# Kernel optimization log

Hardware: AMD Instinct MI355X
Metric: run time of the kernel (lower is better)

## Reference

```python
import jax, jax.numpy as jnp
import numpy as np

B, N, D_MODEL, H = 2, 512, 256, 8
DH, DS, DE = 8, 8, 8          # hyperbolic / spherical / euclidean component dims
HEAD = D_MODEL // H           # 32
HALF = HEAD // 2              # 16 rope frequencies
KAPPA_S = 1.0                 # spherical curvature
EPS = 1e-6


def setup_inputs() -> dict:
    key = jax.random.key(0)
    ks = jax.random.split(key, 10)
    h = jax.random.normal(ks[0], (B, N, D_MODEL), jnp.float32)
    # manifold coords: hyperbolic part inside Poincare ball, spherical part on unit sphere
    xh = 0.3 * jnp.tanh(jax.random.normal(ks[1], (B, N, DH), jnp.float32))
    xs_raw = jax.random.normal(ks[2], (B, N, DS), jnp.float32)
    xs = xs_raw / jnp.linalg.norm(xs_raw, axis=-1, keepdims=True)
    xe = jax.random.normal(ks[3], (B, N, DE), jnp.float32)
    x = jnp.concatenate([xh, xs, xe], axis=-1)
    def lin(k):
        return 0.05 * jax.random.normal(k, (D_MODEL, D_MODEL), jnp.float32)
    inp = dict(
        h=h, x=x,
        Wq=lin(ks[4]), bq=jnp.zeros((D_MODEL,), jnp.float32),
        Wk=lin(ks[5]), bk=jnp.zeros((D_MODEL,), jnp.float32),
        Wv=lin(ks[6]), bv=jnp.zeros((D_MODEL,), jnp.float32),
        Wo=lin(ks[7]), bo=jnp.zeros((D_MODEL,), jnp.float32),
        w_kernel=jnp.ones((H, 3), jnp.float32),   # torch init: ones(num_heads, num_comp)
        beta=jnp.ones((H,), jnp.float32),
        edge_bias=0.1 * jax.random.normal(ks[8], (B, 1, N, N), jnp.float32),
        node_mask=jnp.ones((B, N), bool),
    )
    return inp


def _pairwise_geometry(x):
    """Returns dh (B,N,N), sdot (B,N,N), de2 (B,N,N), dist (B,N,N)."""
    xh, xs, xe = x[..., :DH], x[..., DH:DH + DS], x[..., DH + DS:]
    # hyperbolic: Poincare-ball distance arccosh(1 + 2|a-b|^2 / ((1-|a|^2)(1-|b|^2)))
    dh2_num = jnp.sum((xh[:, :, None, :] - xh[:, None, :, :]) ** 2, -1)
    one_m = 1.0 - jnp.sum(xh * xh, -1)                               # (B,N)
    arg = 1.0 + 2.0 * dh2_num / (one_m[:, :, None] * one_m[:, None, :])
    dh = jnp.arccosh(jnp.maximum(arg, 1.0 + EPS))
    # spherical: arccos of dot (unit vectors); raw dot kept for the kernel term
    sdot = jnp.einsum('bnd,bmd->bnm', xs, xs)
    ds = jnp.arccos(jnp.clip(sdot, -1.0 + EPS, 1.0 - EPS)) / np.sqrt(KAPPA_S)
    # euclidean: squared distance (kernel uses -d^2; product dist uses d^2)
    de2 = jnp.sum((xe[:, :, None, :] - xe[:, None, :, :]) ** 2, -1)
    dist = jnp.sqrt(dh * dh + ds * ds + de2)
    return dh, sdot, de2, dist


def reference(h, x, Wq, bq, Wk, bk, Wv, bv, Wo, bo, w_kernel, beta, edge_bias, node_mask):
    scale = 1.0 / np.sqrt(HEAD)
    rope_freq = jnp.exp(-np.log(10000.0) * jnp.arange(HALF, dtype=jnp.float32) / HALF)

    def heads(t):  # (B,N,D) -> (B,H,N,head)
        return t.reshape(B, N, H, HEAD).transpose(0, 2, 1, 3)

    Q = heads(h @ Wq.T + bq)
    K = heads(h @ Wk.T + bk)
    V = heads(h @ Wv.T + bv)

    dh, sdot, de2, dist = _pairwise_geometry(x)

    # M-RoPE: rotate Q by pairwise angle theta_ij = omega * d_M(x_i, x_j)
    theta = dist[..., None] * rope_freq                  # (B,N,N,half)
    cos_t = jnp.cos(theta)[:, None]                      # (B,1,N,N,half)
    sin_t = jnp.sin(theta)[:, None]
    q1, q2 = Q[..., 0::2], Q[..., 1::2]                  # (B,H,N,half)
    k1, k2 = K[..., 0::2], K[..., 1::2]
    qk_same = q1[:, :, :, None, :] * k1[:, :, None, :, :] + q2[:, :, :, None, :] * k2[:, :, None, :, :]
    qk_cross = q1[:, :, :, None, :] * k2[:, :, None, :, :] - q2[:, :, :, None, :] * k1[:, :, None, :, :]
    attn = (cos_t * qk_same + sin_t * qk_cross).sum(-1) * scale   # (B,H,N,N)

    # geodesic kernel bias: per-component kernels [H:-d_H, S:k*a.b, E:-|a-b|^2]
    kernel_stack = jnp.stack([-dh, KAPPA_S * sdot, -de2], axis=-1)  # (B,N,N,3)
    geo = jnp.einsum('hc,bnmc->bhnm', w_kernel, kernel_stack)
    attn = attn + beta[None, :, None, None] * geo + edge_bias

    attn = jnp.where(node_mask[:, None, None, :], attn, -jnp.inf)
    p = jax.nn.softmax(attn, axis=-1)
    out = jnp.einsum('bhnm,bhmd->bhnd', p, V).transpose(0, 2, 1, 3).reshape(B, N, D_MODEL)
    return out @ Wo.T + bo
```

## Files before the change

### kernel.cpp

```cpp
#include <hip/hip_runtime.h>

#define N_TOK 512
#define NH 8

typedef __attribute__((ext_vector_type(8))) short short8;
typedef __attribute__((ext_vector_type(4))) short short4v;
typedef __attribute__((ext_vector_type(4))) float f32x4;

__device__ __forceinline__ unsigned short f2bf(float f) {
    union { float f; unsigned u; } v; v.f = f;
    return (unsigned short)((v.u + 0x7FFF + ((v.u >> 16) & 1)) >> 16);
}

__global__ __launch_bounds__(256) void gemm_qkv_mfma(
    const float* __restrict__ A,
    const float* __restrict__ Wq, const float* __restrict__ Wk, const float* __restrict__ Wv,
    const float* __restrict__ bq, const float* __restrict__ bk, const float* __restrict__ bv,
    float* __restrict__ Qb, float* __restrict__ KR, float* __restrict__ Vb)
{
    const int bx = blockIdx.x;
    const int t = threadIdx.x;
    const int z = bx >> 8, rem = bx & 255;
    const int m0 = (rem >> 3) * 32, n0 = (rem & 7) * 32;
    const float* W    = (z == 0) ? Wq : (z == 1) ? Wk : Wv;
    const float* bias = (z == 0) ? bq : (z == 1) ? bk : bv;

    __shared__ short As[32][264];
    __shared__ short Ws[32][264];

    #pragma unroll
    for (int r = 0; r < 8; ++r) {
        int idx = t + 256 * r;
        int row = idx >> 6, c4 = (idx & 63) * 4;
        float4 a = *(const float4*)&A[(m0 + row) * 256 + c4];
        short4v pa = {(short)f2bf(a.x), (short)f2bf(a.y), (short)f2bf(a.z), (short)f2bf(a.w)};
        *(short4v*)&As[row][c4] = pa;
        float4 w = *(const float4*)&W[(n0 + row) * 256 + c4];
        short4v pw = {(short)f2bf(w.x), (short)f2bf(w.y), (short)f2bf(w.z), (short)f2bf(w.w)};
        *(short4v*)&Ws[row][c4] = pw;
    }
    __syncthreads();

    const int w = t >> 6, lane = t & 63;
    const int wm = (w >> 1) * 16, wn = (w & 1) * 16;
    const int frow = lane & 15, kq = lane >> 4;

    f32x4 acc = {0.f, 0.f, 0.f, 0.f};
    #pragma unroll
    for (int k0 = 0; k0 < 8; ++k0) {
        short8 af = *(const short8*)&As[wm + frow][k0 * 32 + kq * 8];
        short8 wf = *(const short8*)&Ws[wn + frow][k0 * 32 + kq * 8];
        if (z == 1) acc = __builtin_amdgcn_mfma_f32_16x16x32_bf16(wf, af, acc, 0, 0, 0);
        else        acc = __builtin_amdgcn_mfma_f32_16x16x32_bf16(af, wf, acc, 0, 0, 0);
    }
    const int col = lane & 15, rq = (lane >> 4) * 4;
    if (z == 1) {
        int tok = m0 + wm + col;
        int bb = tok >> 9, j = tok & 511;
        #pragma unroll
        for (int r = 0; r < 4; ++r) {
            int d = n0 + wn + rq + r;
            int h = d >> 5, dd = d & 31, f = dd >> 1, r2 = dd & 1;
            KR[((size_t)bb * 128 + h * 16 + f) * 1024 + j * 2 + r2] = acc[r] + bias[d];
        }
    } else {
        float* C = (z == 0) ? Qb : Vb;
        float bsv = bias[n0 + wn + col];
        #pragma unroll
        for (int r = 0; r < 4; ++r)
            C[(m0 + wm + rq + r) * 256 + n0 + wn + col] = acc[r] + bsv;
    }
}

__global__ __launch_bounds__(256) void geo_kernel(
    const float* __restrict__ x, float* __restrict__ geo)
{
    const int j0 = blockIdx.x * 256;
    const int i  = blockIdx.y;
    const int b  = blockIdx.z;
    const int t  = threadIdx.x;

    __shared__ float xls[256 * 25];
    const float4* xsrc = (const float4*)(x + ((size_t)b * N_TOK + j0) * 24);
    #pragma unroll
    for (int r = 0; r < 6; ++r) {
        int idx = t + 256 * r;
        float4 v = xsrc[idx];
        int row = idx / 6, c = (idx % 6) * 4;
        float* dst = &xls[row * 25 + c];
        dst[0] = v.x; dst[1] = v.y; dst[2] = v.z; dst[3] = v.w;
    }
    const float* xi = x + ((size_t)b * N_TOK + i) * 24;
    float onemi = 1.0f;
    #pragma unroll
    for (int k = 0; k < 8; ++k) onemi -= xi[k] * xi[k];
    __syncthreads();

    const float* xr = &xls[t * 25];
    float dh2 = 0.f, oj = 0.f, sd = 0.f, de2 = 0.f;
    #pragma unroll
    for (int k = 0; k < 8; ++k) { float xj = xr[k]; float d = xi[k] - xj; dh2 += d * d; oj += xj * xj; }
    #pragma unroll
    for (int k = 0; k < 8; ++k) sd += xi[8 + k] * xr[8 + k];
    #pragma unroll
    for (int k = 0; k < 8; ++k) { float d = xi[16 + k] - xr[16 + k]; de2 += d * d; }
    float arg = 1.0f + 2.0f * dh2 / (onemi * (1.0f - oj));
    arg = fmaxf(arg, 1.0f + 1e-6f);
    float dh = __logf(arg + sqrtf(arg * arg - 1.0f));
    float sdc = fminf(fmaxf(sd, -1.0f + 1e-6f), 1.0f - 1e-6f);
    float dsp = acosf(sdc);
    float dist = sqrtf(dh * dh + dsp * dsp + de2);

    size_t idx = ((size_t)b * N_TOK + i) * N_TOK + j0 + t;
    float4 o; o.x = dh; o.y = sd; o.z = de2; o.w = dist * 0.15915494309189535f;
    *(float4*)&geo[idx * 4] = o;
}

__global__ __launch_bounds__(256, 4) void attn_kernel(
    const float* __restrict__ Q, const float* __restrict__ KR, const float* __restrict__ V,
    const float* __restrict__ geo, const float* __restrict__ eb,
    const float* __restrict__ wker, const float* __restrict__ beta,
    float* __restrict__ num, float* __restrict__ den)
{
    const float FRQ[16] = {
        1.0f, 0.5623413251903491f, 0.31622776601683794f, 0.17782794100389228f,
        0.1f, 0.05623413251903491f, 0.031622776601683794f, 0.017782794100389228f,
        0.01f, 0.005623413251903491f, 0.0031622776601683794f, 0.0017782794100389228f,
        0.001f, 0.0005623413251903491f, 0.00031622776601683795f, 0.00017782794100389228f};

    const int t = threadIdx.x;
    const int lane = t & 63;
    const int wv = t >> 6;
    const int wid = blockIdx.x * 4 + wv;
    const int b  = __builtin_amdgcn_readfirstlane(wid >> 12);
    const int h  = __builtin_amdgcn_readfirstlane((wid >> 9) & 7);
    const int ip = __builtin_amdgcn_readfirstlane((wid >> 1) & 255);
    const int jh = __builtin_amdgcn_readfirstlane(wid & 1);
    const int i0 = ip * 2;

    __shared__ float es[4][2][128];

    const float* q0p = Q + ((size_t)b * N_TOK + i0) * 256 + h * 32;
    const float* q1p = q0p + 256;
    const float wk0 = wker[h * 3 + 0], wk1 = wker[h * 3 + 1], wk2 = wker[h * 3 + 2];
    const float bet = beta[h];
    const float scale = 0.17677669529663687f;

    const size_t gbase = ((size_t)b * N_TOK + i0) * N_TOK;
    const float* kbase = KR + ((size_t)b * 128 + h * 16) * 1024;

    float dsum[2] = {0.f, 0.f};
    float acc[2][4] = {{0.f,0.f,0.f,0.f},{0.f,0.f,0.f,0.f}};
    const int jsub = lane >> 3, dq = lane & 7;

    for (int tile = 0; tile < 2; ++tile) {
        const int j0 = jh * 256 + tile * 128;
        float2 gdh[2], gsd[2], gde[2], gds[2];
        #pragma unroll
        for (int ii = 0; ii < 2; ++ii) {
            size_t gi = (gbase + (size_t)ii * N_TOK + j0 + 2 * lane) * 4;
            float4 g0 = *(const float4*)&geo[gi];
            float4 g1 = *(const float4*)&geo[gi + 4];
            gdh[ii] = make_float2(g0.x, g1.x);
            gsd[ii] = make_float2(g0.y, g1.y);
            gde[ii] = make_float2(g0.z, g1.z);
            gds[ii] = make_float2(g0.w, g1.w);
        }
        float dot[2][2] = {{0.f, 0.f}, {0.f, 0.f}};
        #pragma unroll
        for (int fg = 0; fg < 2; ++fg) {
            float4 kv[8];
            #pragma unroll
            for (int fl = 0; fl < 8; ++fl)
                kv[fl] = *(const float4*)&kbase[(size_t)(fg * 8 + fl) * 1024 + (j0 + 2 * lane) * 2];
            #pragma unroll
            for (int fl = 0; fl < 8; ++fl) {
                const int f = fg * 8 + fl;
                const float frq = FRQ[f];
                float4 kk = kv[fl];
                #pragma unroll
                for (int ii = 0; ii < 2; ++ii) {
                    const float* qp = ii ? q1p : q0p;
                    float q1 = qp[f * 2], q2 = qp[f * 2 + 1];
                    float r0 = gds[ii].x * frq; r0 -= floorf(r0);
                    float r1 = gds[ii].y * frq; r1 -= floorf(r1);
                    float s0 = __builtin_amdgcn_sinf(r0), c0 = __builtin_amdgcn_cosf(r0);
                    float s1 = __builtin_amdgcn_sinf(r1), c1 = __builtin_amdgcn_cosf(r1);
                    float t1 = q1 * kk.x + q2 * kk.y;
                    float t2 = q1 * kk.y - q2 * kk.x;
                    dot[ii][0] += c0 * t1 + s0 * t2;
                    t1 = q1 * kk.z + q2 * kk.w;
                    t2 = q1 * kk.w - q2 * kk.z;
                    dot[ii][1] += c1 * t1 + s1 * t2;
                }
            }
        }
        #pragma unroll
        for (int ii = 0; ii < 2; ++ii) {
            float2 e2 = *(const float2*)&eb[((size_t)b * N_TOK + i0 + ii) * N_TOK + j0 + 2 * lane];
            float bias0 = bet * (wk1 * gsd[ii].x - wk0 * gdh[ii].x - wk2 * gde[ii].x) + e2.x;
            float bias1 = bet * (wk1 * gsd[ii].y - wk0 * gdh[ii].y - wk2 * gde[ii].y) + e2.y;
            float e0 = __expf(dot[ii][0] * scale + bias0);
            float e1 = __expf(dot[ii][1] * scale + bias1);
            dsum[ii] += e0 + e1;
            *(float2*)&es[wv][ii][2 * lane] = make_float2(e0, e1);
        }
        {
            const float* vp = V + ((size_t)b * N_TOK + j0 + jsub) * 256 + h * 32 + dq * 4;
            #pragma unroll
            for (int it = 0; it < 16; ++it) {
                float4 v4 = *(const float4*)&vp[(size_t)it * 8 * 256];
                int j = it * 8 + jsub;
                float e0 = es[wv][0][j], e1 = es[wv][1][j];
                acc[0][0] += e0 * v4.x; acc[0][1] += e0 * v4.y;
                acc[0][2] += e0 * v4.z; acc[0][3] += e0 * v4.w;
                acc[1][0] += e1 * v4.x; acc[1][1] += e1 * v4.y;
                acc[1][2] += e1 * v4.z; acc[1][3] += e1 * v4.w;
            }
        }
    }

    #pragma unroll
    for (int ii = 0; ii < 2; ++ii) {
        float v = dsum[ii];
        v += __shfl_xor(v, 1);  v += __shfl_xor(v, 2);  v += __shfl_xor(v, 4);
        v += __shfl_xor(v, 8);  v += __shfl_xor(v, 16); v += __shfl_xor(v, 32);
        dsum[ii] = v;
    }
    #pragma unroll
    for (int ii = 0; ii < 2; ++ii)
        #pragma unroll
        for (int dd = 0; dd < 4; ++dd) {
            float a = acc[ii][dd];
            a += __shfl_xor(a, 8); a += __shfl_xor(a, 16); a += __shfl_xor(a, 32);
            acc[ii][dd] = a;
        }
    float* denp = den + (size_t)jh * 8192;
    if (lane == 0) {
        denp[((size_t)b * N_TOK + i0) * 8 + h]     = dsum[0];
        denp[((size_t)b * N_TOK + i0 + 1) * 8 + h] = dsum[1];
    }
    if (jsub == 0) {
        #pragma unroll
        for (int ii = 0; ii < 2; ++ii) {
            float4 o; o.x = acc[ii][0]; o.y = acc[ii][1]; o.z = acc[ii][2]; o.w = acc[ii][3];
            *(float4*)&num[(size_t)jh * 262144 + ((size_t)b * N_TOK + i0 + ii) * 256 + h * 32 + dq * 4] = o;
        }
    }
}

__global__ __launch_bounds__(256) void gemm_out_mfma(
    const float* __restrict__ num, const float* __restrict__ den,
    const float* __restrict__ Wo, const float* __restrict__ bo, float* __restrict__ out)
{
    const int t = threadIdx.x;
    const int m0 = (blockIdx.x >> 3) * 32, n0 = (blockIdx.x & 7) * 32;

    __shared__ short As[32][264];
    __shared__ short Ws[32][264];

    #pragma unroll
    for (int r = 0; r < 8; ++r) {
        int idx = t + 256 * r;
        int row = idx >> 6, c4 = (idx & 63) * 4;
        int m = m0 + row;
        float4 a0 = *(const float4*)&num[(size_t)m * 256 + c4];
        float4 a1 = *(const float4*)&num[262144 + (size_t)m * 256 + c4];
        int hh = c4 >> 5;
        float dsum = den[m * 8 + hh] + den[8192 + m * 8 + hh];
        float inv = 1.0f / dsum;
        short4v pa = {(short)f2bf((a0.x + a1.x) * inv), (short)f2bf((a0.y + a1.y) * inv),
                      (short)f2bf((a0.z + a1.z) * inv), (short)f2bf((a0.w + a1.w) * inv)};
        *(short4v*)&As[row][c4] = pa;
        float4 w = *(const float4*)&Wo[(n0 + row) * 256 + c4];
        short4v pw = {(short)f2bf(w.x), (short)f2bf(w.y), (short)f2bf(w.z), (short)f2bf(w.w)};
        *(short4v*)&Ws[row][c4] = pw;
    }
    __syncthreads();

    const int w = t >> 6, lane = t & 63;
    const int wm = (w >> 1) * 16, wn = (w & 1) * 16;
    const int frow = lane & 15, kq = lane >> 4;

    f32x4 acc = {0.f, 0.f, 0.f, 0.f};
    #pragma unroll
    for (int k0 = 0; k0 < 8; ++k0) {
        short8 af = *(const short8*)&As[wm + frow][k0 * 32 + kq * 8];
        short8 wf = *(const short8*)&Ws[wn + frow][k0 * 32 + kq * 8];
        acc = __builtin_amdgcn_mfma_f32_16x16x32_bf16(af, wf, acc, 0, 0, 0);
    }
    const int col = lane & 15, rq = (lane >> 4) * 4;
    float bsv = bo[n0 + wn + col];
    #pragma unroll
    for (int r = 0; r < 4; ++r)
        out[(m0 + wm + rq + r) * 256 + n0 + wn + col] = acc[r] + bsv;
}

extern "C" void kernel_launch(void* const* d_in, const int* in_sizes, int n_in,
                              void* d_out, int out_size, void* d_ws, size_t ws_size,
                              hipStream_t stream) {
    const float* hin  = (const float*)d_in[0];
    const float* x    = (const float*)d_in[1];
    const float* Wq   = (const float*)d_in[2];
    const float* bq   = (const float*)d_in[3];
    const float* Wk   = (const float*)d_in[4];
    const float* bk   = (const float*)d_in[5];
    const float* Wv   = (const float*)d_in[6];
    const float* bv   = (const float*)d_in[7];
    const float* Wo   = (const float*)d_in[8];
    const float* bo   = (const float*)d_in[9];
    const float* wker = (const float*)d_in[10];
    const float* beta = (const float*)d_in[11];
    const float* eb   = (const float*)d_in[12];
    float* out = (float*)d_out;
    float* w   = (float*)d_ws;

    float* Qb  = w;
    float* KR  = w + 262144;
    float* Vb  = w + 524288;
    float* num = w + 786432;
    float* den = w + 1310720;
    float* geo = w + 1327104;

    hipLaunchKernelGGL(gemm_qkv_mfma, dim3(768), dim3(256), 0, stream,
                       hin, Wq, Wk, Wv, bq, bk, bv, Qb, KR, Vb);
    hipLaunchKernelGGL(geo_kernel, dim3(2, 512, 2), dim3(256), 0, stream,
                       x, geo);
    hipLaunchKernelGGL(attn_kernel, dim3(2048), dim3(256), 0, stream,
                       Qb, KR, Vb, geo, eb, wker, beta, num, den);
    hipLaunchKernelGGL(gemm_out_mfma, dim3(256), dim3(256), 0, stream,
                       num, den, Wo, bo, out);
}
```

Before: 137.7 us.

## Process four query rows per wave in attention and precompute geo bias early

Each wave in the attention kernel now handles four query rows instead of two, so every K-rotation and V tile load is reused across more rows, and the grid is halved. The block-to-work mapping is changed so the four waves of a block share b, h and the j-half. The geometry bias and edge bias are folded into one value right after loading, using nontemporal loads, which shortens their register lifetime. In exchange the kernel uses more registers and a larger shared buffer, which may reduce occupancy.

```diff
diff --git a/kernel.cpp b/kernel.cpp
--- a/kernel.cpp
+++ b/kernel.cpp
@@ -6,6 +6,7 @@
 typedef __attribute__((ext_vector_type(8))) short short8;
 typedef __attribute__((ext_vector_type(4))) short short4v;
 typedef __attribute__((ext_vector_type(4))) float f32x4;
+typedef __attribute__((ext_vector_type(2))) float f32x2;
 
 __device__ __forceinline__ unsigned short f2bf(float f) {
     union { float f; unsigned u; } v; v.f = f;
@@ -131,17 +132,19 @@
     const int t = threadIdx.x;
     const int lane = t & 63;
     const int wv = t >> 6;
-    const int wid = blockIdx.x * 4 + wv;
-    const int b  = __builtin_amdgcn_readfirstlane(wid >> 12);
-    const int h  = __builtin_amdgcn_readfirstlane((wid >> 9) & 7);
-    const int ip = __builtin_amdgcn_readfirstlane((wid >> 1) & 255);
-    const int jh = __builtin_amdgcn_readfirstlane(wid & 1);
-    const int i0 = ip * 2;
-
-    __shared__ float es[4][2][128];
-
-    const float* q0p = Q + ((size_t)b * N_TOK + i0) * 256 + h * 32;
-    const float* q1p = q0p + 256;
+    const int bx = blockIdx.x;
+    const int b   = __builtin_amdgcn_readfirstlane(bx >> 9);
+    const int h   = __builtin_amdgcn_readfirstlane((bx >> 6) & 7);
+    const int jh  = __builtin_amdgcn_readfirstlane((bx >> 5) & 1);
+    const int ig4 = __builtin_amdgcn_readfirstlane(bx & 31);
+    const int i0  = (ig4 * 4 + wv) * 4;
+
+    __shared__ float es[4][4][128];
+
+    const float* qp0 = Q + ((size_t)b * N_TOK + i0) * 256 + h * 32;
+    const float* qp1 = qp0 + 256;
+    const float* qp2 = qp0 + 512;
+    const float* qp3 = qp0 + 768;
     const float wk0 = wker[h * 3 + 0], wk1 = wker[h * 3 + 1], wk2 = wker[h * 3 + 2];
     const float bet = beta[h];
     const float scale = 0.17677669529663687f;
@@ -149,24 +152,25 @@
     const size_t gbase = ((size_t)b * N_TOK + i0) * N_TOK;
     const float* kbase = KR + ((size_t)b * 128 + h * 16) * 1024;
 
-    float dsum[2] = {0.f, 0.f};
-    float acc[2][4] = {{0.f,0.f,0.f,0.f},{0.f,0.f,0.f,0.f}};
+    float dsum[4] = {0.f, 0.f, 0.f, 0.f};
+    float acc[4][4] = {{0.f,0.f,0.f,0.f},{0.f,0.f,0.f,0.f},{0.f,0.f,0.f,0.f},{0.f,0.f,0.f,0.f}};
     const int jsub = lane >> 3, dq = lane & 7;
 
     for (int tile = 0; tile < 2; ++tile) {
         const int j0 = jh * 256 + tile * 128;
-        float2 gdh[2], gsd[2], gde[2], gds[2];
-        #pragma unroll
-        for (int ii = 0; ii < 2; ++ii) {
+        float2 bias2[4], rev2[4];
+        #pragma unroll
+        for (int ii = 0; ii < 4; ++ii) {
             size_t gi = (gbase + (size_t)ii * N_TOK + j0 + 2 * lane) * 4;
-            float4 g0 = *(const float4*)&geo[gi];
-            float4 g1 = *(const float4*)&geo[gi + 4];
-            gdh[ii] = make_float2(g0.x, g1.x);
-            gsd[ii] = make_float2(g0.y, g1.y);
-            gde[ii] = make_float2(g0.z, g1.z);
-            gds[ii] = make_float2(g0.w, g1.w);
-        }
-        float dot[2][2] = {{0.f, 0.f}, {0.f, 0.f}};
+            f32x4 g0 = __builtin_nontemporal_load((const f32x4*)&geo[gi]);
+            f32x4 g1 = __builtin_nontemporal_load((const f32x4*)&geo[gi + 4]);
+            f32x2 e2 = __builtin_nontemporal_load(
+                (const f32x2*)&eb[((size_t)b * N_TOK + i0 + ii) * N_TOK + j0 + 2 * lane]);
+            bias2[ii].x = bet * (wk1 * g0.y - wk0 * g0.x - wk2 * g0.z) + e2.x;
+            bias2[ii].y = bet * (wk1 * g1.y - wk0 * g1.x - wk2 * g1.z) + e2.y;
+            rev2[ii] = make_float2(g0.w, g1.w);
+        }
+        float dot[4][2] = {{0,0},{0,0},{0,0},{0,0}};
         #pragma unroll
         for (int fg = 0; fg < 2; ++fg) {
             float4 kv[8];
@@ -179,11 +183,11 @@
                 const float frq = FRQ[f];
                 float4 kk = kv[fl];
                 #pragma unroll
-                for (int ii = 0; ii < 2; ++ii) {
-                    const float* qp = ii ? q1p : q0p;
+                for (int ii = 0; ii < 4; ++ii) {
+                    const float* qp = (ii == 0) ? qp0 : (ii == 1) ? qp1 : (ii == 2) ? qp2 : qp3;
                     float q1 = qp[f * 2], q2 = qp[f * 2 + 1];
-                    float r0 = gds[ii].x * frq; r0 -= floorf(r0);
-                    float r1 = gds[ii].y * frq; r1 -= floorf(r1);
+                    float r0 = rev2[ii].x * frq; r0 -= floorf(r0);
+                    float r1 = rev2[ii].y * frq; r1 -= floorf(r1);
                     float s0 = __builtin_amdgcn_sinf(r0), c0 = __builtin_amdgcn_cosf(r0);
                     float s1 = __builtin_amdgcn_sinf(r1), c1 = __builtin_amdgcn_cosf(r1);
                     float t1 = q1 * kk.x + q2 * kk.y;
@@ -196,12 +200,9 @@
             }
         }
         #pragma unroll
-        for (int ii = 0; ii < 2; ++ii) {
-            float2 e2 = *(const float2*)&eb[((size_t)b * N_TOK + i0 + ii) * N_TOK + j0 + 2 * lane];
-            float bias0 = bet * (wk1 * gsd[ii].x - wk0 * gdh[ii].x - wk2 * gde[ii].x) + e2.x;
-            float bias1 = bet * (wk1 * gsd[ii].y - wk0 * gdh[ii].y - wk2 * gde[ii].y) + e2.y;
-            float e0 = __expf(dot[ii][0] * scale + bias0);
-            float e1 = __expf(dot[ii][1] * scale + bias1);
+        for (int ii = 0; ii < 4; ++ii) {
+            float e0 = __expf(dot[ii][0] * scale + bias2[ii].x);
+            float e1 = __expf(dot[ii][1] * scale + bias2[ii].y);
             dsum[ii] += e0 + e1;
             *(float2*)&es[wv][ii][2 * lane] = make_float2(e0, e1);
         }
@@ -211,24 +212,25 @@
             for (int it = 0; it < 16; ++it) {
                 float4 v4 = *(const float4*)&vp[(size_t)it * 8 * 256];
                 int j = it * 8 + jsub;
-                float e0 = es[wv][0][j], e1 = es[wv][1][j];
-                acc[0][0] += e0 * v4.x; acc[0][1] += e0 * v4.y;
-                acc[0][2] += e0 * v4.z; acc[0][3] += e0 * v4.w;
-                acc[1][0] += e1 * v4.x; acc[1][1] += e1 * v4.y;
-                acc[1][2] += e1 * v4.z; acc[1][3] += e1 * v4.w;
+                #pragma unroll
+                for (int ii = 0; ii < 4; ++ii) {
+                    float e = es[wv][ii][j];
+                    acc[ii][0] += e * v4.x; acc[ii][1] += e * v4.y;
+                    acc[ii][2] += e * v4.z; acc[ii][3] += e * v4.w;
+                }
             }
         }
     }
 
     #pragma unroll
-    for (int ii = 0; ii < 2; ++ii) {
+    for (int ii = 0; ii < 4; ++ii) {
         float v = dsum[ii];
         v += __shfl_xor(v, 1);  v += __shfl_xor(v, 2);  v += __shfl_xor(v, 4);
         v += __shfl_xor(v, 8);  v += __shfl_xor(v, 16); v += __shfl_xor(v, 32);
         dsum[ii] = v;
     }
     #pragma unroll
-    for (int ii = 0; ii < 2; ++ii)
+    for (int ii = 0; ii < 4; ++ii)
         #pragma unroll
         for (int dd = 0; dd < 4; ++dd) {
             float a = acc[ii][dd];
@@ -237,12 +239,13 @@
         }
     float* denp = den + (size_t)jh * 8192;
     if (lane == 0) {
-        denp[((size_t)b * N_TOK + i0) * 8 + h]     = dsum[0];
-        denp[((size_t)b * N_TOK + i0 + 1) * 8 + h] = dsum[1];
+        #pragma unroll
+        for (int ii = 0; ii < 4; ++ii)
+            denp[((size_t)b * N_TOK + i0 + ii) * 8 + h] = dsum[ii];
     }
     if (jsub == 0) {
         #pragma unroll
-        for (int ii = 0; ii < 2; ++ii) {
+        for (int ii = 0; ii < 4; ++ii) {
             float4 o; o.x = acc[ii][0]; o.y = acc[ii][1]; o.z = acc[ii][2]; o.w = acc[ii][3];
             *(float4*)&num[(size_t)jh * 262144 + ((size_t)b * N_TOK + i0 + ii) * 256 + h * 32 + dq * 4] = o;
         }
@@ -326,7 +329,7 @@
                        hin, Wq, Wk, Wv, bq, bk, bv, Qb, KR, Vb);
     hipLaunchKernelGGL(geo_kernel, dim3(2, 512, 2), dim3(256), 0, stream,
                        x, geo);
-    hipLaunchKernelGGL(attn_kernel, dim3(2048), dim3(256), 0, stream,
+    hipLaunchKernelGGL(attn_kernel, dim3(1024), dim3(256), 0, stream,
                        Qb, KR, Vb, geo, eb, wker, beta, num, den);
     hipLaunchKernelGGL(gemm_out_mfma, dim3(256), dim3(256), 0, stream,
                        num, den, Wo, bo, out);
```

Measured after the change: 427.9 us. +210.6%, slower.
